# Kernel optimization log

Measured on AMD Instinct MI355X. Metric: run time of the kernel, lower is better.

The kernel has to match this reference:

```python
import jax, jax.numpy as jnp
import numpy as np

SUB_NO, T_NO, T_DATA, E_NO, I_NO, N_BASIS = 20, 200, 50000, 2000, 500, 20


def _make_cos_basis():
    x = np.arange(T_NO, dtype=np.float32)
    raw = 6.0 * np.log(x + 1.0)  # cos_scale=6, cos_shift=1
    basis = np.zeros((N_BASIS, T_NO), np.float32)
    for i in range(N_BASIS):
        phi = 0.5 * np.pi * i
        b = 0.5 * np.cos(raw - phi) + 0.5
        basis[i] = np.where((raw < phi - np.pi) | (raw > phi + np.pi), 0.0, b)
    return basis


def _make_tree():
    C = np.zeros((SUB_NO, SUB_NO), np.int32)
    for p in range(SUB_NO):
        for c in (2 * p + 1, 2 * p + 2):
            if c < SUB_NO:
                C[p, c] = 1
    return C


def _one_hot_assign(n_syn):
    C = np.zeros((SUB_NO, n_syn), np.int32)
    C[np.arange(n_syn) % SUB_NO, np.arange(n_syn)] = 1
    return C


def setup_inputs() -> dict:
    key = jax.random.key(0)
    ks = jax.random.split(key, 12)
    f32 = jnp.float32
    S_e = (jax.random.uniform(ks[0], (T_DATA, E_NO)) < 0.02).astype(f32)
    S_i = (jax.random.uniform(ks[1], (T_DATA, I_NO)) < 0.02).astype(f32)
    Z = (jax.random.uniform(ks[2], (T_DATA,)) < 0.05).astype(f32)
    return {
        "S_e": S_e, "S_i": S_i, "Z": Z,
        "C_den": jnp.asarray(_make_tree()),
        "C_syn_e": jnp.asarray(_one_hot_assign(E_NO)),
        "C_syn_i": jnp.asarray(_one_hot_assign(I_NO)),
        "cos_basis": jnp.asarray(_make_cos_basis()),
        "W_syn": jax.random.normal(ks[3], (SUB_NO, N_BASIS, 2), f32) * 0.1,
        "W_hist": jax.random.normal(ks[4], (N_BASIS,), f32) * 0.1,
        "W_sub": jnp.ones((SUB_NO,), f32) * 0.1,
        "W_spk": jnp.ones((1,), f32),
        "Tau_spk": jnp.ones((1,), f32) * 3.0,
        "V_o": jax.random.normal(ks[5], (1,), f32),
        "Theta": jax.random.normal(ks[6], (SUB_NO,), f32) * 0.1,
        "weight1": jax.random.normal(ks[7], (SUB_NO, 5), f32) * 0.1,
        "weight2": jax.random.normal(ks[8], (SUB_NO, 5, 5), f32) * 0.1,
        "weight3": jax.random.normal(ks[9], (SUB_NO, 5, 5), f32) * 0.1,
        "weight4": jax.random.normal(ks[10], (5, SUB_NO), f32) * 0.1,
    }


def reference(S_e, S_i, Z, C_den, C_syn_e, C_syn_i, cos_basis, W_syn, W_hist,
              W_sub, W_spk, Tau_spk, V_o, Theta, weight1, weight2, weight3, weight4):
    f32 = jnp.float32
    T = S_e.shape[0]
    sub_no = weight1.shape[0]
    T_no = cos_basis.shape[1]
    Cd = C_den.astype(f32)

    # synapse -> subunit projection
    syn_e = S_e @ C_syn_e.astype(f32).T  # [T, sub]
    syn_i = S_i @ C_syn_i.astype(f32).T

    e_kern = W_syn[:, :, 0] @ cos_basis  # [sub, T_no]
    i_kern = W_syn[:, :, 1] @ cos_basis

    def grouped_causal_conv(x, kern):
        # torch: pad T_no-1 zeros in front, grouped conv with flipped kernel (true causal conv)
        xp = jnp.pad(x, ((T_no - 1, 0), (0, 0))).T[None]  # [1, sub, T+T_no-1]
        k = kern[:, None, ::-1]  # [sub, 1, T_no]
        y = jax.lax.conv_general_dilated(xp, k, (1,), 'VALID',
                                         dimension_numbers=('NCH', 'OIH', 'NCH'),
                                         feature_group_count=x.shape[1])
        return y[0].T  # [T, sub]

    syn = grouped_causal_conv(syn_e, e_kern) + grouped_causal_conv(syn_i, i_kern)

    def causal_conv_lag1(z, kern):
        # torch: pad T_no zeros in front, valid conv with flipped kernel, drop last -> [T]
        zp = jnp.pad(z, (T_no, 0))[None, None]  # [1,1,T+T_no]
        k = kern[None, None, ::-1]
        y = jax.lax.conv_general_dilated(zp, k, (1,), 'VALID',
                                         dimension_numbers=('NCH', 'OIH', 'NCH'))
        return y[0, 0, :-1]

    hist_kern = W_hist @ cos_basis  # [T_no]
    hist_filt = causal_conv_lag1(Z, hist_kern)

    lrelu = jax.nn.leaky_relu  # negative_slope 0.01 matches torch default
    W_sub2 = W_sub ** 2

    def sub_mlp(s, x):
        h = lrelu(x[:, None] * weight1[s][None, :])  # [T,5]
        h = lrelu(h @ weight2[s])
        h = lrelu(h @ weight3[s])
        return h @ weight4[:, s]  # [T]

    # tree recurrence: children have higher index, processed last-to-first
    ns_out = jnp.zeros((T, sub_no), f32)
    for s in range(sub_no - 1):
        sub_idx = sub_no - 1 - s
        agg = ns_out @ (Cd[sub_idx] * W_sub2)  # equals gather-leaf weighted sum (0 if leaf)
        ns_in = lrelu(syn[:, sub_idx] + Theta[sub_idx] + agg)
        ns_out = ns_out.at[:, sub_idx].set(sub_mlp(sub_idx, ns_in))

    root_in = lrelu(hist_filt + syn[:, 0] + ns_out @ (Cd[0] * W_sub2) + Theta[0])
    final_Z = jax.nn.sigmoid(sub_mlp(0, root_in))

    t = jnp.arange(T_no, dtype=f32)
    t_tau = t / Tau_spk[0] ** 2
    spk_kern = t_tau * jnp.exp(-t_tau) * W_spk[0] ** 2
    final_V = causal_conv_lag1(Z, spk_kern) + V_o[0]

    out_filters = jnp.concatenate([e_kern, i_kern, hist_kern[None, :]], axis=0)
    return final_V, final_Z, out_filters
```

## Files before the change

kernel.cpp:

```cpp
#include <hip/hip_runtime.h>
#include <math.h>

#define T_DATA 50000
#define SUB_NO 20
#define T_NO 200
#define N_BASIS 20

#define WS_E    0
#define WS_I    1000000
#define WS_EKT  2000000
#define WS_IKT  2004000
#define WS_WSE  2008400
#define WS_HF   2008800

#define KA_RED_BLOCKS 586
#define KA_HIST_BLOCKS 196
#define KA_TOTAL (KA_RED_BLOCKS + 1 + KA_HIST_BLOCKS)

__device__ __forceinline__ float lrelu(float x) { return x > 0.f ? x : 0.01f * x; }

__global__ __launch_bounds__(256) void kA(const float* __restrict__ Se,
                                          const float* __restrict__ Si,
                                          const float* __restrict__ Z,
                                          const int* __restrict__ C_den,
                                          const float* __restrict__ cb,
                                          const float* __restrict__ W_syn,
                                          const float* __restrict__ W_hist,
                                          const float* __restrict__ W_sub,
                                          const float* __restrict__ W_spk,
                                          const float* __restrict__ Tau,
                                          const float* __restrict__ Vo,
                                          float* __restrict__ ws,
                                          float* __restrict__ out) {
    int tid = threadIdx.x;
    int bid = blockIdx.x;

    if (bid < KA_RED_BLOCKS) {
        int gid = bid * 256 + tid;
        if (gid >= T_DATA * 5) return;
        int t = gid / 5, sg = gid % 5;
        const float4* Se4 = (const float4*)Se;
        const float4* Si4 = (const float4*)Si;

        float4 a = make_float4(0.f, 0.f, 0.f, 0.f);
        int base_e = t * 500 + sg;
        #pragma unroll 10
        for (int g = 0; g < 100; g++) {
            float4 v = Se4[base_e + g * 5];
            a.x += v.x; a.y += v.y; a.z += v.z; a.w += v.w;
        }
        float4 b = make_float4(0.f, 0.f, 0.f, 0.f);
        int base_i = t * 125 + sg;
        #pragma unroll
        for (int g = 0; g < 25; g++) {
            float4 v = Si4[base_i + g * 5];
            b.x += v.x; b.y += v.y; b.z += v.z; b.w += v.w;
        }
        ((float4*)(ws + WS_E))[t * 5 + sg] = a;
        ((float4*)(ws + WS_I))[t * 5 + sg] = b;
        return;
    }

    if (bid == KA_RED_BLOCKS) {
        for (int j = tid; j < 4000; j += 256) {
            int s = j / 200, tau = j % 200;
            float se = 0.f, si = 0.f;
            #pragma unroll
            for (int b = 0; b < N_BASIS; b++) {
                float c = cb[b * 200 + tau];
                se += W_syn[(s * N_BASIS + b) * 2 + 0] * c;
                si += W_syn[(s * N_BASIS + b) * 2 + 1] * c;
            }
            ws[WS_EKT + tau * 20 + s] = se;
            ws[WS_IKT + tau * 20 + s] = si;
            out[2 * T_DATA + j] = se;
            out[2 * T_DATA + 4000 + j] = si;
        }
        for (int j = tid; j < 200; j += 256) {
            float h = 0.f;
            #pragma unroll
            for (int b = 0; b < N_BASIS; b++) h += W_hist[b] * cb[b * 200 + j];
            out[2 * T_DATA + 8000 + j] = h;
        }
        for (int j = tid; j < 400; j += 256) {
            int c = j % 20;
            ws[WS_WSE + j] = (float)C_den[j] * W_sub[c] * W_sub[c];
        }
        return;
    }

    __shared__ float z[456];
    __shared__ float2 hk[200];
    int t0 = (bid - KA_RED_BLOCKS - 1) * 256;
    for (int f = tid; f < 456; f += 256) {
        int u = t0 - 200 + f;
        z[f] = (u >= 0 && u < T_DATA) ? Z[u] : 0.f;
    }
    if (tid < 200) {
        float h = 0.f;
        #pragma unroll
        for (int b = 0; b < N_BASIS; b++) h += W_hist[b] * cb[b * 200 + tid];
        float tau2 = Tau[0] * Tau[0];
        float tt = (float)tid / tau2;
        float sk = tt * expf(-tt) * W_spk[0] * W_spk[0];
        hk[tid] = make_float2(h, sk);
    }
    __syncthreads();
    float ha = 0.f, sa = 0.f;
    #pragma unroll 4
    for (int tau = 0; tau < T_NO; tau++) {
        float zv = z[tid + 199 - tau];
        float2 hv = hk[tau];
        ha += zv * hv.x;
        sa += zv * hv.y;
    }
    int t = t0 + tid;
    if (t < T_DATA) {
        out[t] = sa + Vo[0];
        ws[WS_HF + t] = ha;
    }
}

__device__ __forceinline__ float sub_mlp(int s, float x,
                                         const float* __restrict__ w1,
                                         const float* __restrict__ w2,
                                         const float* __restrict__ w3,
                                         const float* __restrict__ w4) {
    float h1[5], h2[5], h3[5];
    #pragma unroll
    for (int k = 0; k < 5; k++) h1[k] = lrelu(x * w1[s * 5 + k]);
    #pragma unroll
    for (int j = 0; j < 5; j++) {
        float v = 0.f;
        #pragma unroll
        for (int k = 0; k < 5; k++) v += h1[k] * w2[s * 25 + k * 5 + j];
        h2[j] = lrelu(v);
    }
    #pragma unroll
    for (int j = 0; j < 5; j++) {
        float v = 0.f;
        #pragma unroll
        for (int k = 0; k < 5; k++) v += h2[k] * w3[s * 25 + k * 5 + j];
        h3[j] = lrelu(v);
    }
    float o = 0.f;
    #pragma unroll
    for (int k = 0; k < 5; k++) o += h3[k] * w4[k * 20 + s];
    return o;
}

#define K3_X 64
#define K3_T 128
#define K3_R (K3_T + 199)

__global__ __launch_bounds__(320) void kB(const float* __restrict__ ws,
                                          const float* __restrict__ Theta,
                                          const float* __restrict__ w1,
                                          const float* __restrict__ w2,
                                          const float* __restrict__ w3,
                                          const float* __restrict__ w4,
                                          float* __restrict__ out) {
    __shared__ float4 tile[2 * 5 * K3_R];
    int x = threadIdx.x;
    int sg = __builtin_amdgcn_readfirstlane(threadIdx.y);
    int t0 = blockIdx.x * K3_T;

    const float4* wsE4 = (const float4*)(ws + WS_E);
    const float4* wsI4 = (const float4*)(ws + WS_I);
    int lin = x + 64 * sg;
    long gbase = (long)(t0 - 199) * 5;
    for (int f = lin; f < K3_R * 5; f += 320) {
        long g = gbase + f;
        int row = f / 5, gg = f % 5;
        float4 ve = make_float4(0.f, 0.f, 0.f, 0.f);
        float4 vi = ve;
        if (g >= 0 && g < (long)T_DATA * 5) {
            ve = wsE4[g];
            vi = wsI4[g];
        }
        tile[(0 * 5 + gg) * K3_R + row] = ve;
        tile[(1 * 5 + gg) * K3_R + row] = vi;
    }
    __syncthreads();

    const float4* eK = (const float4*)(ws + WS_EKT);
    const float4* iK = (const float4*)(ws + WS_IKT);
    float4 acc0 = make_float4(0.f, 0.f, 0.f, 0.f);
    float4 acc1 = acc0;
    const float4* te = &tile[(0 * 5 + sg) * K3_R];
    const float4* ti = &tile[(1 * 5 + sg) * K3_R];

    #pragma unroll 4
    for (int tau = 0; tau < T_NO; tau++) {
        float4 ke = eK[tau * 5 + sg];
        float4 ki = iK[tau * 5 + sg];
        int r = x + 199 - tau;
        float4 e0 = te[r],      i0 = ti[r];
        float4 e1 = te[r + 64], i1 = ti[r + 64];
        acc0.x += e0.x * ke.x + i0.x * ki.x;
        acc0.y += e0.y * ke.y + i0.y * ki.y;
        acc0.z += e0.z * ke.z + i0.z * ki.z;
        acc0.w += e0.w * ke.w + i0.w * ki.w;
        acc1.x += e1.x * ke.x + i1.x * ki.x;
        acc1.y += e1.y * ke.y + i1.y * ki.y;
        acc1.z += e1.z * ke.z + i1.z * ki.z;
        acc1.w += e1.w * ke.w + i1.w * ki.w;
    }

    __syncthreads();
    float4* accL4 = tile;
    accL4[sg * 128 + x] = acc0;
    accL4[sg * 128 + x + 64] = acc1;
    __syncthreads();

    if (sg != 0) return;
    const float* wse = ws + WS_WSE;
    #pragma unroll
    for (int half = 0; half < 2; half++) {
        int t = t0 + x + half * 64;
        if (t >= T_DATA) break;
        int xi = x + half * 64;
        float acc[20];
        #pragma unroll
        for (int g = 0; g < 5; g++) {
            float4 v = accL4[g * 128 + xi];
            acc[g * 4 + 0] = v.x; acc[g * 4 + 1] = v.y;
            acc[g * 4 + 2] = v.z; acc[g * 4 + 3] = v.w;
        }
        float ns[20];
        #pragma unroll
        for (int s = 0; s < 20; s++) ns[s] = 0.f;
        #pragma unroll
        for (int si = 19; si >= 1; si--) {
            float ag = 0.f;
            #pragma unroll
            for (int c = 0; c < 20; c++) ag += wse[si * 20 + c] * ns[c];
            float xx = lrelu(acc[si] + Theta[si] + ag);
            ns[si] = sub_mlp(si, xx, w1, w2, w3, w4);
        }
        float ag0 = 0.f;
        #pragma unroll
        for (int c = 0; c < 20; c++) ag0 += wse[c] * ns[c];
        float x0 = lrelu(ws[WS_HF + t] + acc[0] + ag0 + Theta[0]);
        float zf = sub_mlp(0, x0, w1, w2, w3, w4);
        out[T_DATA + t] = 1.f / (1.f + expf(-zf));
    }
}

extern "C" void kernel_launch(void* const* d_in, const int* in_sizes, int n_in,
                              void* d_out, int out_size, void* d_ws, size_t ws_size,
                              hipStream_t stream) {
    const float* S_e    = (const float*)d_in[0];
    const float* S_i    = (const float*)d_in[1];
    const float* Z      = (const float*)d_in[2];
    const int*   C_den  = (const int*)d_in[3];
    const float* cb     = (const float*)d_in[6];
    const float* W_syn  = (const float*)d_in[7];
    const float* W_hist = (const float*)d_in[8];
    const float* W_sub  = (const float*)d_in[9];
    const float* W_spk  = (const float*)d_in[10];
    const float* Tau    = (const float*)d_in[11];
    const float* V_o    = (const float*)d_in[12];
    const float* Theta  = (const float*)d_in[13];
    const float* w1     = (const float*)d_in[14];
    const float* w2     = (const float*)d_in[15];
    const float* w3     = (const float*)d_in[16];
    const float* w4     = (const float*)d_in[17];
    float* out = (float*)d_out;
    float* ws  = (float*)d_ws;

    kA<<<KA_TOTAL, 256, 0, stream>>>(S_e, S_i, Z, C_den, cb, W_syn, W_hist,
                                     W_sub, W_spk, Tau, V_o, ws, out);
    dim3 b3(K3_X, 5);
    kB<<<(T_DATA + K3_T - 1) / K3_T, b3, 0, stream>>>(
        ws, Theta, w1, w2, w3, w4, out);
}
```

Before: 664.5 us.

## Register-block kB convolution over four time steps with strided shared layout

kB now covers 256 time steps per block instead of 128. Each thread computes four consecutive outputs, using shared memory stored as four strided sub-rows. Sliding-window registers reuse each shared-memory load across four accumulators, cutting LDS reads per FMA. The tree MLP tail now runs on 256 threads (4 waves) instead of one wave, spreading that serial work across more lanes. The trade-offs are higher register pressure and half as many blocks.

```diff
diff --git a/kernel.cpp b/kernel.cpp
--- a/kernel.cpp
+++ b/kernel.cpp
@@ -149,9 +149,10 @@
     return o;
 }
 
-#define K3_X 64
-#define K3_T 128
-#define K3_R (K3_T + 199)
+#define KB_X 64
+#define KB_T 256
+#define KB_ROWS 455
+#define KB_SRP 115
 
 __global__ __launch_bounds__(320) void kB(const float* __restrict__ ws,
                                           const float* __restrict__ Theta,
@@ -160,91 +161,99 @@
                                           const float* __restrict__ w3,
                                           const float* __restrict__ w4,
                                           float* __restrict__ out) {
-    __shared__ float4 tile[2 * 5 * K3_R];
+    __shared__ float4 tile[2 * 5 * 4 * KB_SRP];
     int x = threadIdx.x;
     int sg = __builtin_amdgcn_readfirstlane(threadIdx.y);
-    int t0 = blockIdx.x * K3_T;
+    int t0 = blockIdx.x * KB_T;
+    int lin = x + 64 * sg;
 
     const float4* wsE4 = (const float4*)(ws + WS_E);
     const float4* wsI4 = (const float4*)(ws + WS_I);
-    int lin = x + 64 * sg;
     long gbase = (long)(t0 - 199) * 5;
-    for (int f = lin; f < K3_R * 5; f += 320) {
+    for (int f = lin; f < KB_ROWS * 5; f += 320) {
         long g = gbase + f;
         int row = f / 5, gg = f % 5;
+        int sub = row & 3, idx = row >> 2;
         float4 ve = make_float4(0.f, 0.f, 0.f, 0.f);
         float4 vi = ve;
         if (g >= 0 && g < (long)T_DATA * 5) {
             ve = wsE4[g];
             vi = wsI4[g];
         }
-        tile[(0 * 5 + gg) * K3_R + row] = ve;
-        tile[(1 * 5 + gg) * K3_R + row] = vi;
+        tile[((0 * 5 + gg) * 4 + sub) * KB_SRP + idx] = ve;
+        tile[((1 * 5 + gg) * 4 + sub) * KB_SRP + idx] = vi;
     }
     __syncthreads();
 
     const float4* eK = (const float4*)(ws + WS_EKT);
     const float4* iK = (const float4*)(ws + WS_IKT);
-    float4 acc0 = make_float4(0.f, 0.f, 0.f, 0.f);
-    float4 acc1 = acc0;
-    const float4* te = &tile[(0 * 5 + sg) * K3_R];
-    const float4* ti = &tile[(1 * 5 + sg) * K3_R];
-
-    #pragma unroll 4
-    for (int tau = 0; tau < T_NO; tau++) {
-        float4 ke = eK[tau * 5 + sg];
-        float4 ki = iK[tau * 5 + sg];
-        int r = x + 199 - tau;
-        float4 e0 = te[r],      i0 = ti[r];
-        float4 e1 = te[r + 64], i1 = ti[r + 64];
-        acc0.x += e0.x * ke.x + i0.x * ki.x;
-        acc0.y += e0.y * ke.y + i0.y * ki.y;
-        acc0.z += e0.z * ke.z + i0.z * ki.z;
-        acc0.w += e0.w * ke.w + i0.w * ki.w;
-        acc1.x += e1.x * ke.x + i1.x * ki.x;
-        acc1.y += e1.y * ke.y + i1.y * ki.y;
-        acc1.z += e1.z * ke.z + i1.z * ki.z;
-        acc1.w += e1.w * ke.w + i1.w * ki.w;
+    const float4* te = &tile[(0 * 5 + sg) * 4 * KB_SRP];
+    const float4* ti = &tile[(1 * 5 + sg) * 4 * KB_SRP];
+
+    float4 we[4], wi[4], acc[4];
+    #pragma unroll
+    for (int j = 0; j < 4; j++) acc[j] = make_float4(0.f, 0.f, 0.f, 0.f);
+    we[0] = te[0 * KB_SRP + x + 50]; wi[0] = ti[0 * KB_SRP + x + 50];
+    we[1] = te[1 * KB_SRP + x + 50]; wi[1] = ti[1 * KB_SRP + x + 50];
+    we[2] = te[2 * KB_SRP + x + 50]; wi[2] = ti[2 * KB_SRP + x + 50];
+
+    for (int m = 0; m < 50; m++) {
+        int idx = x + 49 - m;
+        #pragma unroll
+        for (int p = 0; p < 4; p++) {
+            int tau = 4 * m + p;
+            const int s0 = (3 - p) & 3;
+            we[s0] = te[s0 * KB_SRP + idx];
+            wi[s0] = ti[s0 * KB_SRP + idx];
+            float4 ke = eK[tau * 5 + sg];
+            float4 ki = iK[tau * 5 + sg];
+            #pragma unroll
+            for (int j = 0; j < 4; j++) {
+                const int sl = (s0 + j) & 3;
+                acc[j].x += we[sl].x * ke.x + wi[sl].x * ki.x;
+                acc[j].y += we[sl].y * ke.y + wi[sl].y * ki.y;
+                acc[j].z += we[sl].z * ke.z + wi[sl].z * ki.z;
+                acc[j].w += we[sl].w * ke.w + wi[sl].w * ki.w;
+            }
+        }
     }
 
     __syncthreads();
     float4* accL4 = tile;
-    accL4[sg * 128 + x] = acc0;
-    accL4[sg * 128 + x + 64] = acc1;
-    __syncthreads();
-
-    if (sg != 0) return;
+    #pragma unroll
+    for (int j = 0; j < 4; j++) accL4[(sg * 4 + j) * 64 + x] = acc[j];
+    __syncthreads();
+
+    if (lin >= 256) return;
+    int w = lin >> 6, xr = lin & 63;
+    int t = t0 + 4 * xr + w;
+    if (t >= T_DATA) return;
+
+    float acc20[20];
+    #pragma unroll
+    for (int g = 0; g < 5; g++) {
+        float4 v = accL4[(g * 4 + w) * 64 + xr];
+        acc20[g * 4 + 0] = v.x; acc20[g * 4 + 1] = v.y;
+        acc20[g * 4 + 2] = v.z; acc20[g * 4 + 3] = v.w;
+    }
     const float* wse = ws + WS_WSE;
-    #pragma unroll
-    for (int half = 0; half < 2; half++) {
-        int t = t0 + x + half * 64;
-        if (t >= T_DATA) break;
-        int xi = x + half * 64;
-        float acc[20];
-        #pragma unroll
-        for (int g = 0; g < 5; g++) {
-            float4 v = accL4[g * 128 + xi];
-            acc[g * 4 + 0] = v.x; acc[g * 4 + 1] = v.y;
-            acc[g * 4 + 2] = v.z; acc[g * 4 + 3] = v.w;
-        }
-        float ns[20];
-        #pragma unroll
-        for (int s = 0; s < 20; s++) ns[s] = 0.f;
-        #pragma unroll
-        for (int si = 19; si >= 1; si--) {
-            float ag = 0.f;
-            #pragma unroll
-            for (int c = 0; c < 20; c++) ag += wse[si * 20 + c] * ns[c];
-            float xx = lrelu(acc[si] + Theta[si] + ag);
-            ns[si] = sub_mlp(si, xx, w1, w2, w3, w4);
-        }
-        float ag0 = 0.f;
-        #pragma unroll
-        for (int c = 0; c < 20; c++) ag0 += wse[c] * ns[c];
-        float x0 = lrelu(ws[WS_HF + t] + acc[0] + ag0 + Theta[0]);
-        float zf = sub_mlp(0, x0, w1, w2, w3, w4);
-        out[T_DATA + t] = 1.f / (1.f + expf(-zf));
-    }
+    float ns[20];
+    #pragma unroll
+    for (int s = 0; s < 20; s++) ns[s] = 0.f;
+    #pragma unroll
+    for (int si = 19; si >= 1; si--) {
+        float ag = 0.f;
+        #pragma unroll
+        for (int c = 0; c < 20; c++) ag += wse[si * 20 + c] * ns[c];
+        float xx = lrelu(acc20[si] + Theta[si] + ag);
+        ns[si] = sub_mlp(si, xx, w1, w2, w3, w4);
+    }
+    float ag0 = 0.f;
+    #pragma unroll
+    for (int c = 0; c < 20; c++) ag0 += wse[c] * ns[c];
+    float x0 = lrelu(ws[WS_HF + t] + acc20[0] + ag0 + Theta[0]);
+    float zf = sub_mlp(0, x0, w1, w2, w3, w4);
+    out[T_DATA + t] = 1.f / (1.f + expf(-zf));
 }
 
 extern "C" void kernel_launch(void* const* d_in, const int* in_sizes, int n_in,
@@ -271,7 +280,7 @@
 
     kA<<<KA_TOTAL, 256, 0, stream>>>(S_e, S_i, Z, C_den, cb, W_syn, W_hist,
                                      W_sub, W_spk, Tau, V_o, ws, out);
-    dim3 b3(K3_X, 5);
-    kB<<<(T_DATA + K3_T - 1) / K3_T, b3, 0, stream>>>(
+    dim3 b3(KB_X, 5);
+    kB<<<(T_DATA + KB_T - 1) / KB_T, b3, 0, stream>>>(
         ws, Theta, w1, w2, w3, w4, out);
 }
```

After: 644.7 us. 3.0% less time.
